# Performance work log

Measured on AMD Instinct MI355X. Metric: run time of the kernel, lower is better.

## Reference

```python
import jax, jax.numpy as jnp
import numpy as np

B, N, D, FF, L = 32, 1000, 128, 512, 6
EPS = 1e-5  # InstanceNorm1d default eps


def _inorm(x, g, b):
    # InstanceNorm1d on [B, d, N] == normalize over sequence dim N per channel (biased var)
    m = jnp.mean(x, axis=1, keepdims=True)
    v = jnp.var(x, axis=1, keepdims=True)
    return (x - m) / jnp.sqrt(v + EPS) * g + b


def setup_inputs() -> dict:
    key = jax.random.key(0)
    ks = jax.random.split(key, 10)
    s = 0.05
    data = jax.random.normal(ks[0], (B, N, 2), dtype=jnp.float32)
    # negative pairwise distances (module calls it negative_dist)
    dist = -jax.random.uniform(ks[1], (B, N, N), dtype=jnp.float32)
    log_scale = jnp.ones((1,), dtype=jnp.float32)
    We = jax.random.normal(ks[2], (D, 2), dtype=jnp.float32) * s
    be = jnp.zeros((D,), dtype=jnp.float32)
    Wq = jax.random.normal(ks[3], (L, D, D), dtype=jnp.float32) * s
    Wk = jax.random.normal(ks[4], (L, D, D), dtype=jnp.float32) * s
    Wv = jax.random.normal(ks[5], (L, D, D), dtype=jnp.float32) * s
    g1 = jnp.ones((L, D), dtype=jnp.float32)
    b1 = jnp.zeros((L, D), dtype=jnp.float32)
    W1 = jax.random.normal(ks[6], (L, FF, D), dtype=jnp.float32) * s
    bw1 = jnp.zeros((L, FF), dtype=jnp.float32)
    W2 = jax.random.normal(ks[7], (L, D, FF), dtype=jnp.float32) * s
    bw2 = jnp.zeros((L, D), dtype=jnp.float32)
    g2 = jnp.ones((L, D), dtype=jnp.float32)
    b2 = jnp.zeros((L, D), dtype=jnp.float32)
    alpha = jnp.ones((L,), dtype=jnp.float32)  # AFT_dist_alpha per layer
    return dict(data=data, dist=dist, log_scale=log_scale, We=We, be=be,
                Wq=Wq, Wk=Wk, Wv=Wv, g1=g1, b1=b1, W1=W1, bw1=bw1,
                W2=W2, bw2=bw2, g2=g2, b2=b2, alpha=alpha)


def reference(data, dist, log_scale, We, be, Wq, Wk, Wv, g1, b1, W1, bw1, W2, bw2, g2, b2, alpha):
    x = data @ We.T + be  # [B,N,D]
    for i in range(L):
        q = x @ Wq[i].T
        k = x @ Wk[i].T
        v = x @ Wv[i].T
        A = jnp.exp(log_scale[0] * alpha[i] * dist)  # [B,N,N]
        ek = jnp.exp(k)
        bias = jnp.einsum('bnm,bmd->bnd', A, ek * v)
        denom = jnp.einsum('bnm,bmd->bnd', A, ek)
        out = jax.nn.sigmoid(q) * (bias / denom)
        x1 = _inorm(x + out, g1[i], b1[i])
        h = jax.nn.relu(x1 @ W1[i].T + bw1[i]) @ W2[i].T + bw2[i]
        x = _inorm(x1 + h, g2[i], b2[i])
    return x
```

## Files before the change

### kernel.cpp

```cpp
#include <hip/hip_runtime.h>
#include <hip/hip_bf16.h>

typedef __attribute__((ext_vector_type(4))) float f32x4;
typedef __attribute__((ext_vector_type(8))) short bf16x8;
typedef __attribute__((ext_vector_type(4))) short s16x4;

#define LCOUNT 6

static __device__ __forceinline__ unsigned short f2b(float f){
  __hip_bfloat16 h = __float2bfloat16(f);
  return __builtin_bit_cast(unsigned short, h);
}
static __device__ __forceinline__ float b2f(unsigned short u){
  unsigned int x = ((unsigned int)u) << 16;
  return __builtin_bit_cast(float, x);
}
static __device__ __forceinline__ void gl16(const void* g, void* l){
  __builtin_amdgcn_global_load_lds(
      (const __attribute__((address_space(1))) void*)g,
      (__attribute__((address_space(3))) void*)l, 16, 0, 0);
}
static __device__ __forceinline__ f32x4 mfma16(bf16x8 a, bf16x8 b, f32x4 c){
  return __builtin_amdgcn_mfma_f32_16x16x32_bf16(a, b, c, 0, 0, 0);
}

__global__ void k_cvt5(const float* __restrict__ Wq, const float* __restrict__ Wk,
                       const float* __restrict__ Wv, const float* __restrict__ W1,
                       const float* __restrict__ W2,
                       unsigned short* __restrict__ wqb, unsigned short* __restrict__ wkb,
                       unsigned short* __restrict__ wvb, unsigned short* __restrict__ w1b,
                       unsigned short* __restrict__ w2b){
  int i = blockIdx.x*256 + threadIdx.x;
  if (i < 98304) wqb[i] = f2b(Wq[i]);
  else if (i < 196608) wkb[i-98304] = f2b(Wk[i-98304]);
  else if (i < 294912) wvb[i-196608] = f2b(Wv[i-196608]);
  else if (i < 688128) w1b[i-294912] = f2b(W1[i-294912]);
  else w2b[i-688128] = f2b(W2[i-688128]);
}

__global__ void k_cvtdist(const float* __restrict__ dist, unsigned short* __restrict__ db){
  int t = blockIdx.x*256 + threadIdx.x;
  int row = t >> 7, ch = t & 127;
  bf16x8 w;
  if (ch >= 125){
#pragma unroll
    for (int e=0;e<8;e++) w[e] = 0;
  } else {
    const float* p = dist + (size_t)row*1000 + ch*8;
    f32x4 a = *(const f32x4*)p;
    f32x4 b = *(const f32x4*)(p + 4);
#pragma unroll
    for (int e=0;e<4;e++){ w[e] = (short)f2b(a[e]); w[4+e] = (short)f2b(b[e]); }
  }
  *(bf16x8*)&db[(size_t)row*1024 + ch*8] = w;
}

__global__ void k_embed(const float* __restrict__ data, const float* __restrict__ We,
                        const float* __restrict__ be, float* __restrict__ x,
                        unsigned short* __restrict__ xb){
  int idx = blockIdx.x*256 + threadIdx.x;
  int d = idx & 127, bn = idx >> 7;
  float v = data[bn*2]*We[d*2] + data[bn*2+1]*We[d*2+1] + be[d];
  x[idx] = v; xb[idx] = f2b(v);
}

__global__ void k_scale(const float* __restrict__ part, int cnt,
                        const float* __restrict__ g, const float* __restrict__ beta,
                        float* __restrict__ na, float* __restrict__ nc){
  int b = blockIdx.x, d = threadIdx.x;
  float s1 = 0.f, s2 = 0.f;
  for (int c = 0; c < cnt; ++c){
    size_t pi = (((size_t)b*cnt + c)*128 + d)*2;
    s1 += part[pi]; s2 += part[pi+1];
  }
  float mean = s1 * 1e-3f;
  float var  = s2 * 1e-3f - mean*mean;
  float a = g[d] * rsqrtf(var + 1e-5f);
  na[b*128 + d] = a; nc[b*128 + d] = beta[d] - mean*a;
}

__global__ __launch_bounds__(256) void k_fapply(
  const float* __restrict__ x, const float* __restrict__ na,
  const float* __restrict__ nc, float* __restrict__ dout){
  int blk = blockIdx.x, tid = threadIdx.x;
  int b = blk / 125;
  size_t base = (size_t)blk*1024 + tid*4;
  int d0 = (tid*4) & 127;
  f32x4 v = *(const f32x4*)&x[base];
  f32x4 o;
#pragma unroll
  for (int e=0;e<4;e++) o[e] = v[e]*na[b*128 + d0 + e] + nc[b*128 + d0 + e];
  *(f32x4*)&dout[base] = o;
}

template<int NORM>
__global__ __launch_bounds__(256) void k_qkv(
  const unsigned short* __restrict__ xb, const float* __restrict__ x,
  const float* __restrict__ na2, const float* __restrict__ nc2,
  const unsigned short* __restrict__ Wqb, const unsigned short* __restrict__ Wkb,
  const unsigned short* __restrict__ Wvb,
  unsigned short* __restrict__ sigq, unsigned short* __restrict__ Zc)
{
  __shared__ unsigned short LA[2*2048];
  __shared__ unsigned short LB[2][4][256][8];
  __shared__ float sna[128], snc[128];
  int tid = threadIdx.x, wid = tid>>6, lane = tid&63;
  int l15 = lane&15, lg = lane>>4;
  int wm = wid>>1, wn = wid&1;
  int bt = blockIdx.x, b = bt>>4, t = bt&15;
  int kv = blockIdx.y;
  int lrow = t*64 + lane; if (lrow > 999) lrow = 999;
  size_t arow = (size_t)(b*1000 + lrow);

  if (NORM){
    if (tid < 128){ sna[tid] = na2[b*128 + tid]; snc[tid] = nc2[b*128 + tid]; }
    __syncthreads();
  }

  f32x4 zf = {0.f,0.f,0.f,0.f};
  f32x4 acc[2][4], acc2[2][4];
#pragma unroll
  for (int i=0;i<2;i++)
#pragma unroll
    for (int j=0;j<4;j++){ acc[i][j] = zf; acc2[i][j] = zf; }

  auto stage = [&](int kk, int buf){
    int k0 = kk*32;
    if (NORM){
      const float* p = x + arow*128 + k0 + wid*8;
      f32x4 v0 = *(const f32x4*)p;
      f32x4 v1 = *(const f32x4*)(p + 4);
      bf16x8 w;
#pragma unroll
      for (int e=0;e<4;e++){
        int k = k0 + wid*8;
        w[e]   = (short)f2b(v0[e]*sna[k+e]   + snc[k+e]);
        w[4+e] = (short)f2b(v1[e]*sna[k+4+e] + snc[k+4+e]);
      }
      *(bf16x8*)&LA[buf*2048 + wid*512 + lane*8] = w;
    } else {
      gl16(xb + arow*128 + k0 + wid*8, &LA[buf*2048 + wid*512]);
    }
    if (kv == 0){
#pragma unroll
      for (int t2=0;t2<2;++t2){
        int e = wid + t2*4, g2 = e>>1, nb = e&1;
        gl16(Wqb + (size_t)(nb*64+lane)*128 + k0 + g2*8, &LB[buf][g2][nb*64][0]);
      }
    } else {
#pragma unroll
      for (int t2=0;t2<4;++t2){
        int e = wid + t2*4, g2 = e&3, nb = e>>2;
        const unsigned short* src = (nb < 2)
          ? Wkb + (size_t)(nb*64+lane)*128 + k0 + g2*8
          : Wvb + (size_t)((nb-2)*64+lane)*128 + k0 + g2*8;
        gl16(src, &LB[buf][g2][nb*64][0]);
      }
    }
  };
  auto compute = [&](int buf){
    bf16x8 af[2];
#pragma unroll
    for (int i=0;i<2;i++){
      int row = wm*32 + i*16 + l15;
      af[i] = *(const bf16x8*)&LA[buf*2048 + lg*512 + row*8];
    }
#pragma unroll
    for (int j=0;j<4;j++){
      bf16x8 bq = *(const bf16x8*)&LB[buf][lg][wn*64 + j*16 + l15][0];
#pragma unroll
      for (int i=0;i<2;i++) acc[i][j] = mfma16(af[i], bq, acc[i][j]);
      if (kv){
        bf16x8 bv = *(const bf16x8*)&LB[buf][lg][128 + wn*64 + j*16 + l15][0];
#pragma unroll
        for (int i=0;i<2;i++) acc2[i][j] = mfma16(af[i], bv, acc2[i][j]);
      }
    }
  };

  stage(0, 0);
  __syncthreads();
  for (int kk = 0; kk < 4; ++kk){
    int buf = kk & 1;
    if (kk < 3) stage(kk+1, buf^1);
    compute(buf);
    __syncthreads();
  }

#pragma unroll
  for (int i=0;i<2;i++){
    int m4 = t*64 + wm*32 + i*16 + lg*4;
    if (m4 >= 1000) continue;
#pragma unroll
    for (int j=0;j<4;j++){
      int col = wn*64 + j*16 + l15;
      if (kv == 0){
#pragma unroll
        for (int r=0;r<4;r++)
          sigq[(size_t)(b*1000 + m4 + r)*128 + col] = f2b(1.f/(1.f + __expf(-acc[i][j][r])));
      } else {
        s16x4 pv, pk;
#pragma unroll
        for (int r=0;r<4;r++){
          float ek = __expf(acc[i][j][r]);
          pk[r] = (short)f2b(ek);
          pv[r] = (short)f2b(ek * acc2[i][j][r]);
        }
        size_t base = ((size_t)(b*128 + (m4>>3))*256 + col)*8 + ((m4>>2)&1)*4;
        *(s16x4*)&Zc[base] = pv;
        *(s16x4*)&Zc[base + 1024] = pk;
      }
    }
  }
}

template<int NORM, int USE16>
__global__ __launch_bounds__(256) void k_attn(
  const float* __restrict__ dist, const unsigned short* __restrict__ db16,
  const unsigned short* __restrict__ Zc, const unsigned short* __restrict__ sigq,
  float* __restrict__ x, float* __restrict__ partA,
  const float* __restrict__ na2, const float* __restrict__ nc2,
  const float* __restrict__ log_scale, const float* __restrict__ alpha, int layer)
{
  union SM {
    struct { unsigned short A[2][4][64][8]; unsigned short B[2][4][256][8]; } st;
    float den[64][128];
  };
  __shared__ SM sm;
  int tid = threadIdx.x, wid = tid>>6, lane = tid&63;
  int l15 = lane&15, lg = lane>>4;
  int bb = blockIdx.y, t = blockIdx.x, n0 = t*64;
  float sc = log_scale[0]*alpha[layer];
  const unsigned short* Zb = Zc + ((size_t)bb << 18);
  int an = n0 + lane; if (an > 999) an = 999;
  const size_t drow = (size_t)(bb*1000 + an);

  f32x4 zf = {0.f,0.f,0.f,0.f};
  f32x4 acc[4][4];
#pragma unroll
  for (int i=0;i<4;i++)
#pragma unroll
    for (int j=0;j<4;j++) acc[i][j] = zf;

  auto issueB = [&](int kk, int buf){
#pragma unroll
    for (int t2=0;t2<4;++t2){
      int e = wid + t2*4, g2 = e&3, cb = e>>2;
      gl16(Zb + ((size_t)((kk*4 + g2)*256 + cb*64 + lane))*8, &sm.st.B[buf][g2][cb*64][0]);
    }
  };
  auto loadA = [&](int kk, float* v){
    int k0 = kk*32 + wid*8;
    if (USE16){
      bf16x8 r = *(const bf16x8*)(db16 + drow*1024 + k0);
#pragma unroll
      for (int e=0;e<8;e++) v[e] = b2f((unsigned short)r[e]);
    } else {
      const float* dp = dist + drow*1000;
      if (k0 + 8 <= 1000){
        f32x4 a0 = *(const f32x4*)(dp + k0);
        f32x4 a1 = *(const f32x4*)(dp + k0 + 4);
#pragma unroll
        for (int e=0;e<4;e++){ v[e] = a0[e]; v[4+e] = a1[e]; }
      } else {
#pragma unroll
        for (int e=0;e<8;e++){
          int m = k0 + e; if (m > 999) m = 999;
          v[e] = dp[m];
        }
      }
    }
  };
  auto expwrite = [&](const float* v, int buf){
    bf16x8 w;
#pragma unroll
    for (int e=0;e<8;e++) w[e] = (short)f2b(__expf(sc*v[e]));
    *(bf16x8*)&sm.st.A[buf][wid][lane][0] = w;
  };
  auto compute = [&](int buf){
    bf16x8 af[4], bq[4];
#pragma unroll
    for (int i=0;i<4;i++) af[i] = *(const bf16x8*)&sm.st.A[buf][lg][i*16 + l15][0];
#pragma unroll
    for (int j=0;j<4;j++) bq[j] = *(const bf16x8*)&sm.st.B[buf][lg][wid*64 + j*16 + l15][0];
#pragma unroll
    for (int i=0;i<4;i++)
#pragma unroll
      for (int j=0;j<4;j++)
        acc[i][j] = mfma16(af[i], bq[j], acc[i][j]);
  };

  float av[8];
  issueB(0, 0);
  loadA(0, av);
  expwrite(av, 0);
  __syncthreads();
  for (int kk = 0; kk < 32; ++kk){
    int buf = kk & 1;
    float nv[8];
    if (kk < 31){ issueB(kk+1, buf^1); loadA(kk+1, nv); }
    compute(buf);
    if (kk < 31) expwrite(nv, buf^1);
    __syncthreads();
  }

  if (wid >= 2){
#pragma unroll
    for (int i=0;i<4;i++)
#pragma unroll
      for (int j=0;j<4;j++){
        int dcol = (wid-2)*64 + j*16 + l15;
#pragma unroll
        for (int r=0;r<4;r++)
          sm.den[i*16 + lg*4 + r][dcol] = acc[i][j][r];
      }
  }
  __syncthreads();
  if (wid < 2){
    float nav[4], ncv[4];
    if (NORM){
#pragma unroll
      for (int j=0;j<4;j++){
        int d = wid*64 + j*16 + l15;
        nav[j] = na2[bb*128 + d]; ncv[j] = nc2[bb*128 + d];
      }
    }
    float s1[4] = {0.f,0.f,0.f,0.f}, s2[4] = {0.f,0.f,0.f,0.f};
#pragma unroll
    for (int i=0;i<4;i++){
#pragma unroll
      for (int r=0;r<4;r++){
        int n = n0 + i*16 + lg*4 + r;
        if (n < 1000){
          size_t rowi = ((size_t)bb*1000 + n)*128;
#pragma unroll
          for (int j=0;j<4;j++){
            int d = wid*64 + j*16 + l15;
            float xv = x[rowi + d];
            if (NORM) xv = xv*nav[j] + ncv[j];
            float y = xv + b2f(sigq[rowi + d]) * acc[i][j][r] / sm.den[i*16 + lg*4 + r][d];
            x[rowi + d] = y;
            s1[j] += y; s2[j] += y*y;
          }
        }
      }
    }
#pragma unroll
    for (int j=0;j<4;j++){
      s1[j] += __shfl_xor(s1[j], 16); s2[j] += __shfl_xor(s2[j], 16);
      s1[j] += __shfl_xor(s1[j], 32); s2[j] += __shfl_xor(s2[j], 32);
    }
    if (lg == 0){
#pragma unroll
      for (int j=0;j<4;j++){
        int d = wid*64 + j*16 + l15;
        size_t pi = (((size_t)bb*16 + t)*128 + d)*2;
        partA[pi] = s1[j]; partA[pi+1] = s2[j];
      }
    }
  }
}

__global__ __launch_bounds__(512) void k_ff1(
  const float* __restrict__ x, const float* __restrict__ partA,
  const float* __restrict__ g1, const float* __restrict__ b1,
  const unsigned short* __restrict__ W1b, const float* __restrict__ bw1,
  float* __restrict__ x1, unsigned short* __restrict__ h1)
{
  __shared__ unsigned short LA[2][4][64][8];
  __shared__ unsigned short LB[2][4][512][8];
  __shared__ float sna[128], snc[128];
  int tid = threadIdx.x, wid = tid>>6, lane = tid&63;
  int l15 = lane&15, lg = lane>>4;
  int wm = wid>>2, wn = wid&3;
  int bt = blockIdx.x, b = bt>>4, t = bt&15;

  if (tid < 128){
    float s1 = 0.f, s2 = 0.f;
    for (int c = 0; c < 16; ++c){
      size_t pi = (((size_t)b*16 + c)*128 + tid)*2;
      s1 += partA[pi]; s2 += partA[pi+1];
    }
    float mean = s1 * 1e-3f;
    float var  = s2 * 1e-3f - mean*mean;
    float a = g1[tid] * rsqrtf(var + 1e-5f);
    sna[tid] = a; snc[tid] = b1[tid] - mean*a;
  }
  __syncthreads();

  f32x4 zf = {0.f,0.f,0.f,0.f};
  f32x4 acc[2][8];
#pragma unroll
  for (int i=0;i<2;i++)
#pragma unroll
    for (int j=0;j<8;j++) acc[i][j] = zf;

  auto stage = [&](int kk, int buf){
    int k0 = kk*32;
    if (tid < 256){
      int row = tid & 63, g2 = tid >> 6;
      int lr = t*64 + row;
      int rr = lr > 999 ? 999 : lr;
      const float* p = x + ((size_t)(b*1000 + rr))*128 + k0 + g2*8;
      f32x4 v0 = *(const f32x4*)p;
      f32x4 v1 = *(const f32x4*)(p + 4);
      f32x4 o0, o1;
      bf16x8 w;
#pragma unroll
      for (int e=0;e<4;e++){
        int k = k0 + g2*8;
        o0[e] = v0[e]*sna[k+e]   + snc[k+e];
        o1[e] = v1[e]*sna[k+4+e] + snc[k+4+e];
        w[e]   = (short)f2b(o0[e]);
        w[4+e] = (short)f2b(o1[e]);
      }
      *(bf16x8*)&LA[buf][g2][row][0] = w;
      if (lr < 1000){
        float* q = x1 + ((size_t)(b*1000 + lr))*128 + k0 + g2*8;
        *(f32x4*)q = o0; *(f32x4*)(q+4) = o1;
      }
    }
#pragma unroll
    for (int t2=0;t2<4;++t2){
      int e = wid*4 + t2;
      int g2 = e & 3, nb = e >> 2;
      gl16(W1b + (size_t)(nb*64 + lane)*128 + k0 + g2*8, &LB[buf][g2][nb*64][0]);
    }
  };
  auto compute = [&](int buf){
    bf16x8 af[2];
#pragma unroll
    for (int i=0;i<2;i++) af[i] = *(const bf16x8*)&LA[buf][lg][wm*32 + i*16 + l15][0];
#pragma unroll
    for (int j=0;j<8;j++){
      bf16x8 bq = *(const bf16x8*)&LB[buf][lg][wn*128 + j*16 + l15][0];
#pragma unroll
      for (int i=0;i<2;i++) acc[i][j] = mfma16(af[i], bq, acc[i][j]);
    }
  };

  stage(0, 0);
  __syncthreads();
  for (int kk = 0; kk < 4; ++kk){
    int buf = kk & 1;
    if (kk < 3) stage(kk+1, buf^1);
    compute(buf);
    __syncthreads();
  }

#pragma unroll
  for (int i=0;i<2;i++){
    int m4 = t*64 + wm*32 + i*16 + lg*4;
    if (m4 >= 1000) continue;
#pragma unroll
    for (int j=0;j<8;j++){
      int col = wn*128 + j*16 + l15;
      float bz = bw1[col];
#pragma unroll
      for (int r=0;r<4;r++){
        float v = acc[i][j][r] + bz;
        h1[(size_t)(b*1000 + m4 + r)*512 + col] = f2b(v > 0.f ? v : 0.f);
      }
    }
  }
}

__global__ __launch_bounds__(256) void k_ff2(
  const unsigned short* __restrict__ h1, const unsigned short* __restrict__ W2b,
  const float* __restrict__ bw2, const float* __restrict__ x1,
  float* __restrict__ x, float* __restrict__ partF)
{
  __shared__ unsigned short LA[2][4][64][8];
  __shared__ unsigned short LB[2][4][128][8];
  int tid = threadIdx.x, wid = tid>>6, lane = tid&63;
  int l15 = lane&15, lg = lane>>4;
  int wm = wid>>1, wn = wid&1;
  int bt = blockIdx.x, b = bt>>4, t = bt&15;
  int lrow = t*64 + lane; if (lrow > 999) lrow = 999;
  size_t arow = (size_t)(b*1000 + lrow);

  f32x4 zf = {0.f,0.f,0.f,0.f};
  f32x4 acc[2][4];
#pragma unroll
  for (int i=0;i<2;i++)
#pragma unroll
    for (int j=0;j<4;j++) acc[i][j] = zf;

  auto stage = [&](int kk, int buf){
    int k0 = kk*32;
    gl16(h1 + arow*512 + k0 + wid*8, &LA[buf][wid][0][0]);
#pragma unroll
    for (int t2=0;t2<2;++t2){
      int e = wid + t2*4, g2 = e>>1, nb = e&1;
      gl16(W2b + (size_t)(nb*64 + lane)*512 + k0 + g2*8, &LB[buf][g2][nb*64][0]);
    }
  };
  auto compute = [&](int buf){
    bf16x8 af[2];
#pragma unroll
    for (int i=0;i<2;i++) af[i] = *(const bf16x8*)&LA[buf][lg][wm*32 + i*16 + l15][0];
#pragma unroll
    for (int j=0;j<4;j++){
      bf16x8 bq = *(const bf16x8*)&LB[buf][lg][wn*64 + j*16 + l15][0];
#pragma unroll
      for (int i=0;i<2;i++) acc[i][j] = mfma16(af[i], bq, acc[i][j]);
    }
  };

  stage(0, 0);
  __syncthreads();
  for (int kk = 0; kk < 16; ++kk){
    int buf = kk & 1;
    if (kk < 15) stage(kk+1, buf^1);
    compute(buf);
    __syncthreads();
  }

  float s1[4] = {0.f,0.f,0.f,0.f}, s2[4] = {0.f,0.f,0.f,0.f};
#pragma unroll
  for (int i=0;i<2;i++){
    int m4 = t*64 + wm*32 + i*16 + lg*4;
    if (m4 >= 1000) continue;
#pragma unroll
    for (int j=0;j<4;j++){
      int col = wn*64 + j*16 + l15;
      float bz = bw2[col];
#pragma unroll
      for (int r=0;r<4;r++){
        size_t idx = (size_t)(b*1000 + m4 + r)*128 + col;
        float y = acc[i][j][r] + bz + x1[idx];
        x[idx] = y;
        s1[j] += y; s2[j] += y*y;
      }
    }
  }
#pragma unroll
  for (int j=0;j<4;j++){
    s1[j] += __shfl_xor(s1[j], 16); s2[j] += __shfl_xor(s2[j], 16);
    s1[j] += __shfl_xor(s1[j], 32); s2[j] += __shfl_xor(s2[j], 32);
  }
  if (lg == 0){
#pragma unroll
    for (int j=0;j<4;j++){
      int d = wn*64 + j*16 + l15;
      size_t pi = (((size_t)b*32 + t*2 + wm)*128 + d)*2;
      partF[pi] = s1[j]; partF[pi+1] = s2[j];
    }
  }
}

extern "C" void kernel_launch(void* const* d_in, const int* in_sizes, int n_in,
                              void* d_out, int out_size, void* d_ws, size_t ws_size,
                              hipStream_t stream) {
  const float* data = (const float*)d_in[0];
  const float* dist = (const float*)d_in[1];
  const float* log_scale = (const float*)d_in[2];
  const float* We = (const float*)d_in[3];
  const float* be = (const float*)d_in[4];
  const float* Wq = (const float*)d_in[5];
  const float* Wk = (const float*)d_in[6];
  const float* Wv = (const float*)d_in[7];
  const float* g1 = (const float*)d_in[8];
  const float* b1 = (const float*)d_in[9];
  const float* W1 = (const float*)d_in[10];
  const float* bw1 = (const float*)d_in[11];
  const float* W2 = (const float*)d_in[12];
  const float* bw2 = (const float*)d_in[13];
  const float* g2 = (const float*)d_in[14];
  const float* b2 = (const float*)d_in[15];
  const float* alpha = (const float*)d_in[16];
  float* dout = (float*)d_out;

  char* ws = (char*)d_ws;
  size_t off = 0;
  auto alloc = [&](size_t bytes) -> void* {
    void* p = ws + off; off += (bytes + 255) & ~(size_t)255; return p;
  };
  unsigned short* xb  = (unsigned short*)alloc(8192000);
  float* x            = (float*)alloc(16384000);
  unsigned short* sigq= (unsigned short*)alloc(8192000);
  unsigned short* Zc  = (unsigned short*)alloc(16777216);
  unsigned short* h1  = (unsigned short*)alloc(32768000);
  float* x1           = (float*)alloc(16384000);
  float* partA        = (float*)alloc(524288);
  float* partF        = (float*)alloc(1048576);
  float* na2          = (float*)alloc(16384);
  float* nc2          = (float*)alloc(16384);
  unsigned short* wqb = (unsigned short*)alloc(196608);
  unsigned short* wkb = (unsigned short*)alloc(196608);
  unsigned short* wvb = (unsigned short*)alloc(196608);
  unsigned short* w1b = (unsigned short*)alloc(786432);
  unsigned short* w2b = (unsigned short*)alloc(786432);
  if (off > ws_size) return;
  unsigned short* db16p = nullptr;
  if (ws_size >= off + 131072256) db16p = (unsigned short*)alloc(131072000);

  hipMemsetAsync(Zc, 0, 16777216, stream);
  k_cvt5<<<4224, 256, 0, stream>>>(Wq, Wk, Wv, W1, W2, wqb, wkb, wvb, w1b, w2b);
  if (db16p) k_cvtdist<<<16000, 256, 0, stream>>>(dist, db16p);
  k_embed<<<16000, 256, 0, stream>>>(data, We, be, x, xb);

  for (int i = 0; i < LCOUNT; ++i){
    if (i > 0)
      k_scale<<<32, 128, 0, stream>>>(partF, 32, g2 + (i-1)*128, b2 + (i-1)*128, na2, nc2);
    if (i == 0)
      k_qkv<0><<<dim3(512,2), 256, 0, stream>>>(xb, x, nullptr, nullptr,
                                                wqb + i*16384, wkb + i*16384, wvb + i*16384,
                                                sigq, Zc);
    else
      k_qkv<1><<<dim3(512,2), 256, 0, stream>>>(nullptr, x, na2, nc2,
                                                wqb + i*16384, wkb + i*16384, wvb + i*16384,
                                                sigq, Zc);
    if (i == 0){
      if (db16p) k_attn<0,1><<<dim3(16,32), 256, 0, stream>>>(dist, db16p, Zc, sigq, x, partA,
                                                              nullptr, nullptr, log_scale, alpha, i);
      else       k_attn<0,0><<<dim3(16,32), 256, 0, stream>>>(dist, nullptr, Zc, sigq, x, partA,
                                                              nullptr, nullptr, log_scale, alpha, i);
    } else {
      if (db16p) k_attn<1,1><<<dim3(16,32), 256, 0, stream>>>(dist, db16p, Zc, sigq, x, partA,
                                                              na2, nc2, log_scale, alpha, i);
      else       k_attn<1,0><<<dim3(16,32), 256, 0, stream>>>(dist, nullptr, Zc, sigq, x, partA,
                                                              na2, nc2, log_scale, alpha, i);
    }
    k_ff1<<<512, 512, 0, stream>>>(x, partA, g1 + i*128, b1 + i*128,
                                   w1b + i*65536, bw1 + i*512, x1, h1);
    k_ff2<<<512, 256, 0, stream>>>(h1, w2b + i*65536, bw2 + i*128, x1, x, partF);
  }
  k_scale<<<32, 128, 0, stream>>>(partF, 32, g2 + 5*128, b2 + 5*128, na2, nc2);
  k_fapply<<<4000, 256, 0, stream>>>(x, na2, nc2, dout);
}
```

Before: 845.2 us.

## Split attention tile across eight waves with 2x4 wave grid

The attention kernel moves from 256 to 512 threads per block, so each wave computes a 32x64 output sub-tile instead of 64x64, halving accumulator registers per wave. Only the first 256 threads load and exponentiate the dist tile, while all waves share the Z staging work. Partial instance-norm statistics are now written per half-tile, so partA doubles and k_ff1 reduces over 32 partials. The intent is more waves in flight to hide memory latency on the dist stream, at the cost of half the threads idling during the A-tile loads and more per-block synchronisation.

```diff
diff --git a/kernel.cpp b/kernel.cpp
--- a/kernel.cpp
+++ b/kernel.cpp
@@ -215,7 +215,7 @@
 }
 
 template<int NORM, int USE16>
-__global__ __launch_bounds__(256) void k_attn(
+__global__ __launch_bounds__(512) void k_attn(
   const float* __restrict__ dist, const unsigned short* __restrict__ db16,
   const unsigned short* __restrict__ Zc, const unsigned short* __restrict__ sigq,
   float* __restrict__ x, float* __restrict__ partA,
@@ -229,28 +229,31 @@
   __shared__ SM sm;
   int tid = threadIdx.x, wid = tid>>6, lane = tid&63;
   int l15 = lane&15, lg = lane>>4;
+  int wm = wid>>2, wn = wid&3;
   int bb = blockIdx.y, t = blockIdx.x, n0 = t*64;
   float sc = log_scale[0]*alpha[layer];
   const unsigned short* Zb = Zc + ((size_t)bb << 18);
-  int an = n0 + lane; if (an > 999) an = 999;
+  int arow_l = tid & 63;
+  int achunk = (tid >> 6) & 3;
+  int an = n0 + arow_l; if (an > 999) an = 999;
   const size_t drow = (size_t)(bb*1000 + an);
 
   f32x4 zf = {0.f,0.f,0.f,0.f};
-  f32x4 acc[4][4];
-#pragma unroll
-  for (int i=0;i<4;i++)
+  f32x4 acc[2][4];
+#pragma unroll
+  for (int i=0;i<2;i++)
 #pragma unroll
     for (int j=0;j<4;j++) acc[i][j] = zf;
 
   auto issueB = [&](int kk, int buf){
 #pragma unroll
-    for (int t2=0;t2<4;++t2){
-      int e = wid + t2*4, g2 = e&3, cb = e>>2;
+    for (int t2=0;t2<2;++t2){
+      int e = wid*2 + t2, g2 = e&3, cb = e>>2;
       gl16(Zb + ((size_t)((kk*4 + g2)*256 + cb*64 + lane))*8, &sm.st.B[buf][g2][cb*64][0]);
     }
   };
   auto loadA = [&](int kk, float* v){
-    int k0 = kk*32 + wid*8;
+    int k0 = kk*32 + achunk*8;
     if (USE16){
       bf16x8 r = *(const bf16x8*)(db16 + drow*1024 + k0);
 #pragma unroll
@@ -275,16 +278,16 @@
     bf16x8 w;
 #pragma unroll
     for (int e=0;e<8;e++) w[e] = (short)f2b(__expf(sc*v[e]));
-    *(bf16x8*)&sm.st.A[buf][wid][lane][0] = w;
+    *(bf16x8*)&sm.st.A[buf][achunk][arow_l][0] = w;
   };
   auto compute = [&](int buf){
-    bf16x8 af[4], bq[4];
-#pragma unroll
-    for (int i=0;i<4;i++) af[i] = *(const bf16x8*)&sm.st.A[buf][lg][i*16 + l15][0];
-#pragma unroll
-    for (int j=0;j<4;j++) bq[j] = *(const bf16x8*)&sm.st.B[buf][lg][wid*64 + j*16 + l15][0];
-#pragma unroll
-    for (int i=0;i<4;i++)
+    bf16x8 af[2], bq[4];
+#pragma unroll
+    for (int i=0;i<2;i++) af[i] = *(const bf16x8*)&sm.st.A[buf][lg][wm*32 + i*16 + l15][0];
+#pragma unroll
+    for (int j=0;j<4;j++) bq[j] = *(const bf16x8*)&sm.st.B[buf][lg][wn*64 + j*16 + l15][0];
+#pragma unroll
+    for (int i=0;i<2;i++)
 #pragma unroll
       for (int j=0;j<4;j++)
         acc[i][j] = mfma16(af[i], bq[j], acc[i][j]);
@@ -292,53 +295,56 @@
 
   float av[8];
   issueB(0, 0);
-  loadA(0, av);
-  expwrite(av, 0);
+  if (tid < 256){ loadA(0, av); expwrite(av, 0); }
   __syncthreads();
   for (int kk = 0; kk < 32; ++kk){
     int buf = kk & 1;
     float nv[8];
-    if (kk < 31){ issueB(kk+1, buf^1); loadA(kk+1, nv); }
+    if (kk < 31){
+      issueB(kk+1, buf^1);
+      if (tid < 256) loadA(kk+1, nv);
+    }
     compute(buf);
-    if (kk < 31) expwrite(nv, buf^1);
+    if (kk < 31 && tid < 256) expwrite(nv, buf^1);
     __syncthreads();
   }
 
-  if (wid >= 2){
-#pragma unroll
-    for (int i=0;i<4;i++)
+  if (wn >= 2){
+#pragma unroll
+    for (int i=0;i<2;i++)
 #pragma unroll
       for (int j=0;j<4;j++){
-        int dcol = (wid-2)*64 + j*16 + l15;
+        int dcol = (wn-2)*64 + j*16 + l15;
 #pragma unroll
         for (int r=0;r<4;r++)
-          sm.den[i*16 + lg*4 + r][dcol] = acc[i][j][r];
+          sm.den[wm*32 + i*16 + lg*4 + r][dcol] = acc[i][j][r];
       }
   }
   __syncthreads();
-  if (wid < 2){
+  if (wn < 2){
     float nav[4], ncv[4];
     if (NORM){
 #pragma unroll
       for (int j=0;j<4;j++){
-        int d = wid*64 + j*16 + l15;
+        int d = wn*64 + j*16 + l15;
         nav[j] = na2[bb*128 + d]; ncv[j] = nc2[bb*128 + d];
       }
     }
     float s1[4] = {0.f,0.f,0.f,0.f}, s2[4] = {0.f,0.f,0.f,0.f};
 #pragma unroll
-    for (int i=0;i<4;i++){
+    for (int i=0;i<2;i++){
 #pragma unroll
       for (int r=0;r<4;r++){
-        int n = n0 + i*16 + lg*4 + r;
+        int lr = wm*32 + i*16 + lg*4 + r;
+        int n = n0 + lr;
         if (n < 1000){
           size_t rowi = ((size_t)bb*1000 + n)*128;
 #pragma unroll
           for (int j=0;j<4;j++){
-            int d = wid*64 + j*16 + l15;
+            int d = wn*64 + j*16 + l15;
             float xv = x[rowi + d];
             if (NORM) xv = xv*nav[j] + ncv[j];
-            float y = xv + b2f(sigq[rowi + d]) * acc[i][j][r] / sm.den[i*16 + lg*4 + r][d];
+            float y = xv + b2f(sigq[rowi + d]) * acc[i][j][r] / sm.den[lr][d];
             x[rowi + d] = y;
             s1[j] += y; s2[j] += y*y;
           }
@@ -353,8 +359,8 @@
     if (lg == 0){
 #pragma unroll
       for (int j=0;j<4;j++){
-        int d = wid*64 + j*16 + l15;
-        size_t pi = (((size_t)bb*16 + t)*128 + d)*2;
+        int d = wn*64 + j*16 + l15;
+        size_t pi = (((size_t)bb*32 + t*2 + wm)*128 + d)*2;
         partA[pi] = s1[j]; partA[pi+1] = s2[j];
       }
     }
@@ -377,8 +383,8 @@
 
   if (tid < 128){
     float s1 = 0.f, s2 = 0.f;
-    for (int c = 0; c < 16; ++c){
-      size_t pi = (((size_t)b*16 + c)*128 + tid)*2;
+    for (int c = 0; c < 32; ++c){
+      size_t pi = (((size_t)b*32 + c)*128 + tid)*2;
       s1 += partA[pi]; s2 += partA[pi+1];
     }
     float mean = s1 * 1e-3f;
@@ -582,7 +588,7 @@
   unsigned short* Zc  = (unsigned short*)alloc(16777216);
   unsigned short* h1  = (unsigned short*)alloc(32768000);
   float* x1           = (float*)alloc(16384000);
-  float* partA        = (float*)alloc(524288);
+  float* partA        = (float*)alloc(1048576);
   float* partF        = (float*)alloc(1048576);
   float* na2          = (float*)alloc(16384);
   float* nc2          = (float*)alloc(16384);
@@ -612,14 +618,14 @@
                                                 wqb + i*16384, wkb + i*16384, wvb + i*16384,
                                                 sigq, Zc);
     if (i == 0){
-      if (db16p) k_attn<0,1><<<dim3(16,32), 256, 0, stream>>>(dist, db16p, Zc, sigq, x, partA,
+      if (db16p) k_attn<0,1><<<dim3(16,32), 512, 0, stream>>>(dist, db16p, Zc, sigq, x, partA,
                                                               nullptr, nullptr, log_scale, alpha, i);
-      else       k_attn<0,0><<<dim3(16,32), 256, 0, stream>>>(dist, nullptr, Zc, sigq, x, partA,
+      else       k_attn<0,0><<<dim3(16,32), 512, 0, stream>>>(dist, nullptr, Zc, sigq, x, partA,
                                                               nullptr, nullptr, log_scale, alpha, i);
     } else {
-      if (db16p) k_attn<1,1><<<dim3(16,32), 256, 0, stream>>>(dist, db16p, Zc, sigq, x, partA,
+      if (db16p) k_attn<1,1><<<dim3(16,32), 512, 0, stream>>>(dist, db16p, Zc, sigq, x, partA,
                                                               na2, nc2, log_scale, alpha, i);
-      else       k_attn<1,0><<<dim3(16,32), 256, 0, stream>>>(dist, nullptr, Zc, sigq, x, partA,
+      else       k_attn<1,0><<<dim3(16,32), 512, 0, stream>>>(dist, nullptr, Zc, sigq, x, partA,
                                                               na2, nc2, log_scale, alpha, i);
     }
     k_ff1<<<512, 512, 0, stream>>>(x, partA, g1 + i*128, b1 + i*128,
```

Result: slower. 901.1 us (+6.6%).
